# Optimization experiments

Measured on AMD Instinct MI355X. Metric: run time of the kernel, lower is better.

## Reference

```python
import jax, jax.numpy as jnp
import numpy as np

B, G = 32, 8          # batch, num_genres
N, T = 64, 64         # notes_size, timestep_size (input)
D, O = 32, 32         # notes_out, timestep_out (output)


def setup_inputs() -> dict:
    key = jax.random.key(0)
    k1, k2, k3, k4, k5 = jax.random.split(key, 5)
    x = jax.random.normal(k1, (B, N, T), dtype=jnp.float32)
    y = jax.random.uniform(k2, (B, G), dtype=jnp.float32)
    weight = jax.random.normal(k3, (G, D, O, N, T), dtype=jnp.float32) * 0.02
    bias = jax.random.normal(k4, (D * O,), dtype=jnp.float32) * 0.02
    mask = jax.random.randint(k5, (O, T), 0, 2).astype(jnp.float32)
    return {"x": x, "y": y, "weight": weight, "bias": bias, "mask": mask}


def reference(x, y, weight, bias, mask):
    # Fused form of:
    #   mw  = einsum('gdont,ot->gdont', weight, mask)
    #   mw2 = einsum('gdont,bg->bdont', mw, y)      # huge intermediate avoided
    #   out = einsum('bnt,bdont->bdo', x, mw2) + bias
    mw = weight * mask[None, None, :, None, :]          # (g,d,o,n,t)
    xw = jnp.einsum('bnt,gdont->bgdo', x, mw)           # contract n,t first
    out = jnp.einsum('bg,bgdo->bdo', y, xw)             # (b,d,o)
    return out + bias.reshape(D, O)[None, :, :]
```

## Files before the change

kernel.cpp:

```cpp
#include <hip/hip_runtime.h>
#include <hip/hip_bf16.h>

typedef __bf16 bf16x8 __attribute__((ext_vector_type(8)));
typedef float f32x4 __attribute__((ext_vector_type(4)));

#define G 8
#define B 32
#define D 32
#define O 32
#define K 4096
#define T 64
#define KSPLIT 2
#define KCHUNK (K / KSPLIT)
#define BK 256
#define NSTEP (KCHUNK / BK)

#define XB_ELEMS (B * K)
#define S_ELEMS  (KSPLIT * G * D * O * B)

__global__ __launch_bounds__(256) void prep_xb(const float* __restrict__ x,
                                               __bf16* __restrict__ xb) {
    int tid = blockIdx.x * 256 + threadIdx.x;
    int kt = tid >> 7;
    int b  = (tid >> 2) & 31;
    int c  = tid & 3;
    int k  = kt * 32 + c * 8;
    const float4 x0 = *(const float4*)(x + b * K + k);
    const float4 x1 = *(const float4*)(x + b * K + k + 4);
    bf16x8 r;
    r[0] = (__bf16)x0.x; r[1] = (__bf16)x0.y; r[2] = (__bf16)x0.z; r[3] = (__bf16)x0.w;
    r[4] = (__bf16)x1.x; r[5] = (__bf16)x1.y; r[6] = (__bf16)x1.z; r[7] = (__bf16)x1.w;
    *(bf16x8*)(xb + (size_t)tid * 8) = r;
}

__global__ __launch_bounds__(256) void gemm_main(const float* __restrict__ W,
                                                 const __bf16* __restrict__ xb,
                                                 const float* __restrict__ mask,
                                                 float* __restrict__ S) {
    __shared__ float ldsW[2][32 * BK];
    const int d  = blockIdx.x, g = blockIdx.y, ks = blockIdx.z;
    const int wid  = threadIdx.x >> 6;
    const int lane = threadIdx.x & 63;
    const int bh = wid & 1, oh = wid >> 1;
    const int l15 = lane & 15, g16 = lane >> 4;

    const int r = oh * 16 + l15;
    const int lds_ro = r * 1024 + ((g16 * 32) ^ ((r & 7) * 16));

    const float* mrow = mask + r * T + g16 * 8;
    const float4 me0 = *(const float4*)(mrow);
    const float4 me1 = *(const float4*)(mrow + 4);
    const float4 mo0 = *(const float4*)(mrow + 32);
    const float4 mo1 = *(const float4*)(mrow + 36);

    const __bf16* xbl = xb + (size_t)(ks * (KCHUNK / 32)) * 1024
                           + (bh * 16 + l15) * 32 + g16 * 8;

    const size_t wrow0 = ((size_t)(g * D + d) * O + 8 * wid) * K + (size_t)ks * KCHUNK;

    f32x4 acc = {0.f, 0.f, 0.f, 0.f};

#define STAGE(buf, step)                                                          \
    {                                                                             \
        _Pragma("unroll")                                                         \
        for (int i = 0; i < 8; ++i) {                                             \
            const int row = 8 * wid + i;                                          \
            const char* src = (const char*)(W + wrow0 + (size_t)i * K             \
                                            + (size_t)(step) * BK)                \
                              + ((lane * 16) ^ (i * 16));                         \
            __builtin_amdgcn_global_load_lds(                                     \
                (const __attribute__((address_space(1))) void*)src,               \
                (__attribute__((address_space(3))) void*)((char*)&ldsW[buf][0]    \
                                                          + row * 1024),          \
                16, 0, 0);                                                        \
        }                                                                         \
    }

    STAGE(0, 0);

    #pragma unroll
    for (int step = 0; step < NSTEP; ++step) {
        const int cur = step & 1;
        if (step + 1 < NSTEP) {
            STAGE(cur ^ 1, step + 1);
            asm volatile("s_waitcnt vmcnt(8)" ::: "memory");
        } else {
            asm volatile("s_waitcnt vmcnt(0)" ::: "memory");
        }
        __builtin_amdgcn_s_barrier();
        asm volatile("" ::: "memory");
        __builtin_amdgcn_sched_barrier(0);

        const char* lb = (const char*)&ldsW[cur][0];
        const __bf16* xs = xbl + (size_t)(step * 8) * 1024;
        #pragma unroll
        for (int s = 0; s < 8; ++s) {
            const int a0 = lds_ro + s * 128;
            const f32x4 alo = *(const f32x4*)(lb + a0);
            const f32x4 ahi = *(const f32x4*)(lb + (a0 ^ 16));
            const float4 ms0 = (s & 1) ? mo0 : me0;
            const float4 ms1 = (s & 1) ? mo1 : me1;
            bf16x8 af;
            af[0] = (__bf16)(alo[0] * ms0.x); af[1] = (__bf16)(alo[1] * ms0.y);
            af[2] = (__bf16)(alo[2] * ms0.z); af[3] = (__bf16)(alo[3] * ms0.w);
            af[4] = (__bf16)(ahi[0] * ms1.x); af[5] = (__bf16)(ahi[1] * ms1.y);
            af[6] = (__bf16)(ahi[2] * ms1.z); af[7] = (__bf16)(ahi[3] * ms1.w);
            const bf16x8 bfr = *(const bf16x8*)(xs + (size_t)s * 1024);
            acc = __builtin_amdgcn_mfma_f32_16x16x32_bf16(af, bfr, acc, 0, 0, 0);
        }

        asm volatile("" ::: "memory");
        __builtin_amdgcn_sched_barrier(0);
        __builtin_amdgcn_s_barrier();
    }
#undef STAGE

    float* Sp = S + (((size_t)(ks * G + g) * D + d) * O + oh * 16) * B + bh * 16;
    #pragma unroll
    for (int i = 0; i < 4; ++i)
        Sp[(g16 * 4 + i) * B + l15] = acc[i];
}

__global__ __launch_bounds__(256) void reduce_out(const float* __restrict__ S,
                                                  const float* __restrict__ y,
                                                  const float* __restrict__ bias,
                                                  float* __restrict__ out) {
    int tid = blockIdx.x * 256 + threadIdx.x;
    int d = tid >> 10, o = (tid >> 5) & 31, b = tid & 31;
    float acc = bias[d * O + o];
    #pragma unroll
    for (int g = 0; g < G; ++g) {
        float s = S[(size_t)g * (D * O * B) + tid]
                + S[(size_t)(G + g) * (D * O * B) + tid];
        acc += y[b * G + g] * s;
    }
    out[b * (D * O) + d * O + o] = acc;
}

extern "C" void kernel_launch(void* const* d_in, const int* in_sizes, int n_in,
                              void* d_out, int out_size, void* d_ws, size_t ws_size,
                              hipStream_t stream) {
    const float* x    = (const float*)d_in[0];
    const float* y    = (const float*)d_in[1];
    const float* w    = (const float*)d_in[2];
    const float* bias = (const float*)d_in[3];
    const float* mask = (const float*)d_in[4];
    float* out = (float*)d_out;

    __bf16* xbp = (__bf16*)d_ws;
    float*  S   = (float*)((char*)d_ws + (size_t)XB_ELEMS * sizeof(__bf16));

    prep_xb<<<64, 256, 0, stream>>>(x, xbp);
    gemm_main<<<dim3(D, G, KSPLIT), 256, 0, stream>>>(w, xbp, mask, S);
    reduce_out<<<128, 256, 0, stream>>>(S, y, bias, out);
}
```

Baseline: 37.94 us.

## Move K-split into the block with 512 threads and prefetch x into registers

The inter-block K split is replaced by an intra-block split: each 512-thread block covers all of K with two wave groups, one per K half, each writing its own partial slab of S. The LDS tile doubles to BK=512 and every stage loads 512-element rows in two 256-element chunks. The x fragments for the next step are now prefetched into registers alongside the weight staging, so global loads of x no longer sit on the MFMA path. In exchange the grid has half as many blocks (256 instead of 512), and the block uses more LDS and registers, which can lower occupancy.

```diff
diff --git a/kernel.cpp b/kernel.cpp
--- a/kernel.cpp
+++ b/kernel.cpp
@@ -10,13 +10,11 @@
 #define O 32
 #define K 4096
 #define T 64
-#define KSPLIT 2
-#define KCHUNK (K / KSPLIT)
-#define BK 256
-#define NSTEP (KCHUNK / BK)
+#define BK 512
+#define NSTEP (K / BK)
 
 #define XB_ELEMS (B * K)
-#define S_ELEMS  (KSPLIT * G * D * O * B)
+#define S_ELEMS  (2 * G * D * O * B)
 
 __global__ __launch_bounds__(256) void prep_xb(const float* __restrict__ x,
                                                __bf16* __restrict__ xb) {
@@ -33,19 +31,20 @@
     *(bf16x8*)(xb + (size_t)tid * 8) = r;
 }
 
-__global__ __launch_bounds__(256) void gemm_main(const float* __restrict__ W,
+__global__ __launch_bounds__(512) void gemm_main(const float* __restrict__ W,
                                                  const __bf16* __restrict__ xb,
                                                  const float* __restrict__ mask,
                                                  float* __restrict__ S) {
     __shared__ float ldsW[2][32 * BK];
-    const int d  = blockIdx.x, g = blockIdx.y, ks = blockIdx.z;
+    const int d = blockIdx.x, g = blockIdx.y;
     const int wid  = threadIdx.x >> 6;
     const int lane = threadIdx.x & 63;
-    const int bh = wid & 1, oh = wid >> 1;
+    const int q = wid & 3, h = wid >> 2;
+    const int bh = q & 1, oh = q >> 1;
     const int l15 = lane & 15, g16 = lane >> 4;
 
     const int r = oh * 16 + l15;
-    const int lds_ro = r * 1024 + ((g16 * 32) ^ ((r & 7) * 16));
+    const int lds_ro = r * 2048 + h * 1024 + ((g16 * 32) ^ ((r & 7) * 16));
 
     const float* mrow = mask + r * T + g16 * 8;
     const float4 me0 = *(const float4*)(mrow);
@@ -53,46 +52,59 @@
     const float4 mo0 = *(const float4*)(mrow + 32);
     const float4 mo1 = *(const float4*)(mrow + 36);
 
-    const __bf16* xbl = xb + (size_t)(ks * (KCHUNK / 32)) * 1024
-                           + (bh * 16 + l15) * 32 + g16 * 8;
+    const __bf16* xbl = xb + (size_t)(h * 8) * 1024 + (bh * 16 + l15) * 32 + g16 * 8;
 
-    const size_t wrow0 = ((size_t)(g * D + d) * O + 8 * wid) * K + (size_t)ks * KCHUNK;
+    const size_t wrow0 = ((size_t)(g * D + d) * O + 4 * wid) * K;
 
     f32x4 acc = {0.f, 0.f, 0.f, 0.f};
 
 #define STAGE(buf, step)                                                          \
     {                                                                             \
         _Pragma("unroll")                                                         \
-        for (int i = 0; i < 8; ++i) {                                             \
-            const int row = 8 * wid + i;                                          \
-            const char* src = (const char*)(W + wrow0 + (size_t)i * K             \
-                                            + (size_t)(step) * BK)                \
-                              + ((lane * 16) ^ (i * 16));                         \
-            __builtin_amdgcn_global_load_lds(                                     \
-                (const __attribute__((address_space(1))) void*)src,               \
-                (__attribute__((address_space(3))) void*)((char*)&ldsW[buf][0]    \
-                                                          + row * 1024),          \
-                16, 0, 0);                                                        \
+        for (int i = 0; i < 4; ++i) {                                             \
+            const int row = 4 * wid + i;                                          \
+            _Pragma("unroll")                                                     \
+            for (int c = 0; c < 2; ++c) {                                         \
+                const char* src = (const char*)(W + wrow0 + (size_t)i * K         \
+                                                + (size_t)(step) * BK + c * 256)  \
+                                  + ((lane * 16) ^ ((row & 7) * 16));             \
+                __builtin_amdgcn_global_load_lds(                                 \
+                    (const __attribute__((address_space(1))) void*)src,           \
+                    (__attribute__((address_space(3))) void*)((char*)&ldsW[buf][0]\
+                                                   + row * 2048 + c * 1024),      \
+                    16, 0, 0);                                                    \
+            }                                                                     \
         }                                                                         \
     }
 
+    bf16x8 xr[2][8];
+#define XLOAD(buf, step)                                                          \
+    {                                                                             \
+        _Pragma("unroll")                                                         \
+        for (int s = 0; s < 8; ++s)                                               \
+            xr[buf][s] = *(const bf16x8*)(xbl + (size_t)(step) * 16384            \
+                                              + (size_t)s * 1024);                \
+    }
+
     STAGE(0, 0);
+    XLOAD(0, 0);
 
     #pragma unroll
     for (int step = 0; step < NSTEP; ++step) {
         const int cur = step & 1;
         if (step + 1 < NSTEP) {
             STAGE(cur ^ 1, step + 1);
-            asm volatile("s_waitcnt vmcnt(8)" ::: "memory");
+            XLOAD(cur ^ 1, step + 1);
+            __builtin_amdgcn_sched_barrier(0);
+            asm volatile("s_waitcnt vmcnt(16)" ::: "memory");
         } else {
+            __builtin_amdgcn_sched_barrier(0);
             asm volatile("s_waitcnt vmcnt(0)" ::: "memory");
         }
         __builtin_amdgcn_s_barrier();
-        asm volatile("" ::: "memory");
         __builtin_amdgcn_sched_barrier(0);
 
         const char* lb = (const char*)&ldsW[cur][0];
-        const __bf16* xs = xbl + (size_t)(step * 8) * 1024;
         #pragma unroll
         for (int s = 0; s < 8; ++s) {
             const int a0 = lds_ro + s * 128;
@@ -105,17 +117,16 @@
             af[2] = (__bf16)(alo[2] * ms0.z); af[3] = (__bf16)(alo[3] * ms0.w);
             af[4] = (__bf16)(ahi[0] * ms1.x); af[5] = (__bf16)(ahi[1] * ms1.y);
             af[6] = (__bf16)(ahi[2] * ms1.z); af[7] = (__bf16)(ahi[3] * ms1.w);
-            const bf16x8 bfr = *(const bf16x8*)(xs + (size_t)s * 1024);
-            acc = __builtin_amdgcn_mfma_f32_16x16x32_bf16(af, bfr, acc, 0, 0, 0);
+            acc = __builtin_amdgcn_mfma_f32_16x16x32_bf16(af, xr[cur][s], acc, 0, 0, 0);
         }
 
         asm volatile("" ::: "memory");
-        __builtin_amdgcn_sched_barrier(0);
         __builtin_amdgcn_s_barrier();
     }
 #undef STAGE
+#undef XLOAD
 
-    float* Sp = S + (((size_t)(ks * G + g) * D + d) * O + oh * 16) * B + bh * 16;
+    float* Sp = S + (((size_t)(h * G + g) * D + d) * O + oh * 16) * B + bh * 16;
     #pragma unroll
     for (int i = 0; i < 4; ++i)
         Sp[(g16 * 4 + i) * B + l15] = acc[i];
@@ -151,6 +162,6 @@
     float*  S   = (float*)((char*)d_ws + (size_t)XB_ELEMS * sizeof(__bf16));
 
     prep_xb<<<64, 256, 0, stream>>>(x, xbp);
-    gemm_main<<<dim3(D, G, KSPLIT), 256, 0, stream>>>(w, xbp, mask, S);
+    gemm_main<<<dim3(D, G), 512, 0, stream>>>(w, xbp, mask, S);
     reduce_out<<<128, 256, 0, stream>>>(S, y, bias, out);
 }
```

Measured after the change: 42.82 us. +12.9%, slower.
